# Kernel optimization log

Measured on AMD Instinct MI355X. Metric: run time of the kernel, lower is better.

## Reference

```python
import jax, jax.numpy as jnp
import numpy as np

D_MODEL = 1024
NUM_HEADS = 16
ROPE_THETA = 10000.0


def setup_inputs() -> dict:
    key = jax.random.key(0)
    ks = jax.random.split(key, 5)
    B, S, D = 4, 2048, D_MODEL
    std = (2.0 / (D * D)) ** 0.5
    return {
        "x": jax.random.normal(ks[0], (B, S, D), dtype=jnp.float32),
        "Wq": jax.random.normal(ks[1], (D, D), dtype=jnp.float32) * std,
        "Wk": jax.random.normal(ks[2], (D, D), dtype=jnp.float32) * std,
        "Wv": jax.random.normal(ks[3], (D, D), dtype=jnp.float32) * std,
        "Wo": jax.random.normal(ks[4], (D, D), dtype=jnp.float32) * std,
    }


def _apply_rope(t, sin, cos):
    # t: [B, H, S, d_k]; sin/cos: [S, d_k//2] (broadcast over B, H)
    e = t[..., 0::2]
    o = t[..., 1::2]
    rot = jnp.stack((e * cos - o * sin, e * sin + o * cos), axis=-1)
    return rot.reshape(t.shape)  # interleave back to d_k


def reference(x, Wq, Wk, Wv, Wo):
    B, S, D = x.shape
    H = NUM_HEADS
    dk = D // H

    def proj(W):
        y = jnp.einsum('bsd,ed->bse', x, W)  # Linear: weight is [out, in]
        return y.reshape(B, S, H, dk).transpose(0, 2, 1, 3)  # [B,H,S,dk]

    q, k, v = proj(Wq), proj(Wk), proj(Wv)

    # RoPE cache (token_positions = arange(S))
    half = dk // 2
    inv_freq = 1.0 / (ROPE_THETA ** (jnp.arange(half, dtype=jnp.float32) * 2.0 / dk))
    angles = jnp.arange(S, dtype=jnp.float32)[:, None] * inv_freq[None, :]  # [S, half]
    sin, cos = jnp.sin(angles), jnp.cos(angles)
    q = _apply_rope(q, sin, cos)
    k = _apply_rope(k, sin, cos)

    # scaled dot-product attention with causal mask
    scores = jnp.einsum('bhqd,bhkd->bhqk', q, k) / jnp.sqrt(jnp.float32(dk))
    causal = jnp.tril(jnp.ones((S, S), dtype=bool))
    scores = jnp.where(causal, scores, jnp.finfo(scores.dtype).min)
    p = jax.nn.softmax(scores, axis=-1)
    out = jnp.einsum('bhqk,bhkd->bhqd', p, v)  # [B,H,S,dk]

    out = out.transpose(0, 2, 1, 3).reshape(B, S, D)
    return jnp.einsum('bsd,ed->bse', out, Wo)
```

## Files before the change

### kernel.cpp

```cpp
#include <hip/hip_runtime.h>

typedef unsigned short u16;
typedef unsigned int   u32;

typedef short    short8 __attribute__((ext_vector_type(8)));
typedef __bf16   bf16x8 __attribute__((ext_vector_type(8)));
typedef _Float16 half8  __attribute__((ext_vector_type(8)));
typedef float    f32x4  __attribute__((ext_vector_type(4)));

#define S_LEN   2048
#define DM      1024
#define NHEAD   16
#define DK      64
#define BH_TOT  64
#define M_TOK   8192
#define KDIM    1024

__device__ __forceinline__ u16 f2bf(float f) {
    u32 u = __builtin_bit_cast(u32, f);
    u += 0x7FFFu + ((u >> 16) & 1u);
    return (u16)(u >> 16);
}
__device__ __forceinline__ f32x4 mfma_bf16(short8 a, short8 b, f32x4 c) {
    return __builtin_amdgcn_mfma_f32_16x16x32_bf16(
        __builtin_bit_cast(bf16x8, a), __builtin_bit_cast(bf16x8, b), c, 0, 0, 0);
}
__device__ __forceinline__ f32x4 mfma_f16(half8 a, half8 b, f32x4 c) {
    return __builtin_amdgcn_mfma_f32_16x16x32_f16(a, b, c, 0, 0, 0);
}
__device__ __forceinline__ u32 pk_f16(float a, float b) {
    return __builtin_bit_cast(u32, __builtin_amdgcn_cvt_pkrtz(a, b));
}
__device__ __forceinline__ void gl_lds16(const void* g, void* l) {
    __builtin_amdgcn_global_load_lds(
        (const __attribute__((address_space(1))) u32*)g,
        (__attribute__((address_space(3))) u32*)l, 16, 0, 0);
}
__device__ __forceinline__ void bar_raw() { asm volatile("s_barrier" ::: "memory"); }
__device__ __forceinline__ void wait_vm4() { asm volatile("s_waitcnt vmcnt(4)" ::: "memory"); }
__device__ __forceinline__ void wait_vm0() { asm volatile("s_waitcnt vmcnt(0)" ::: "memory"); }

__device__ __forceinline__ int perm_inv(int rc) {
    const int nt = rc >> 4, mid = (rc >> 2) & 3, r = rc & 3;
    return 32 * (nt >> 1) + 8 * mid + 4 * (nt & 1) + r;
}

__global__ void cvt_all(const float4* __restrict__ x,  const float4* __restrict__ Wq,
                        const float4* __restrict__ Wk, const float4* __restrict__ Wv,
                        const float4* __restrict__ Wo,
                        uint2* __restrict__ oX, uint2* __restrict__ oWcat,
                        uint2* __restrict__ oWo,
                        float* __restrict__ sT, float* __restrict__ cT) {
    const int i = blockIdx.x * 256 + threadIdx.x;
    if (i < 3145728) {
        const float4* in;
        uint2* out;
        if (i < 2097152) {
            in = x + i;  out = oX + i;
        } else {
            const int j = i - 2097152;
            const int w = j >> 18, k = j & 262143;
            in  = (w == 0 ? Wq : w == 1 ? Wk : w == 2 ? Wv : Wo) + k;
            out = (w < 3) ? (oWcat + w * 262144 + k) : (oWo + k);
        }
        float4 f = *in;
        uint2 o;
        o.x = (u32)f2bf(f.x) | ((u32)f2bf(f.y) << 16);
        o.y = (u32)f2bf(f.z) | ((u32)f2bf(f.w) << 16);
        *out = o;
    } else {
        const int idx = i - 3145728;
        const float fi = expf(-(float)(idx >> 11) * 0.287823136624255f);
        const float ang = (float)(idx & 2047) * fi;
        sT[idx] = sinf(ang);
        cT[idx] = cosf(ang);
    }
}

template <int MODE>
__global__ __launch_bounds__(256)
void gemm_nt(const u16* __restrict__ A, const u16* __restrict__ Bw,
             u16* __restrict__ oQ, u16* __restrict__ oK, u16* __restrict__ oVt,
             float* __restrict__ oF,
             const float* __restrict__ ropeS, const float* __restrict__ ropeC) {
    __shared__ u16 As[2][128 * 32];
    __shared__ u16 Bs[2][128 * 32];
    const int tid  = threadIdx.x;
    const int wave = tid >> 6, lane = tid & 63;
    const int quad = lane >> 4, l15 = lane & 15;
    const int wr = wave >> 1, wc = wave & 1;
    const int mbase = blockIdx.y * 128;
    const int nbase = blockIdx.x * 128;

    f32x4 acc[4][4];
#pragma unroll
    for (int i = 0; i < 4; i++)
#pragma unroll
        for (int j = 0; j < 4; j++) acc[i][j] = (f32x4)0.0f;

    const int srow0 = wave * 32 + (lane >> 2);
    const int srow1 = srow0 + 16;
    const int scolb = ((lane & 3) ^ ((lane >> 3) & 3)) * 16;
    const int ldsOff = wave * 2048 + lane * 16;
    const u16* gA0 = A  + (size_t)(mbase + srow0) * KDIM;
    const u16* gA1 = A  + (size_t)(mbase + srow1) * KDIM;
    const u16* gB0 = Bw + (size_t)(nbase + srow0) * KDIM;
    const u16* gB1 = Bw + (size_t)(nbase + srow1) * KDIM;
    const int koffq = (quad ^ ((l15 >> 1) & 3)) * 8;

    gl_lds16((const char*)gA0 + scolb, (char*)As[0] + ldsOff);
    gl_lds16((const char*)gA1 + scolb, (char*)As[0] + ldsOff + 1024);
    gl_lds16((const char*)gB0 + scolb, (char*)Bs[0] + ldsOff);
    gl_lds16((const char*)gB1 + scolb, (char*)Bs[0] + ldsOff + 1024);

    const int KT = KDIM / 32;
    for (int kt = 0; kt < KT; kt++) {
        const int cur = kt & 1, nxt = cur ^ 1;
        const int kkn = ((kt + 1 < KT) ? (kt + 1) : kt) * 32;
        bar_raw();
        gl_lds16((const char*)(gA0 + kkn) + scolb, (char*)As[nxt] + ldsOff);
        gl_lds16((const char*)(gA1 + kkn) + scolb, (char*)As[nxt] + ldsOff + 1024);
        gl_lds16((const char*)(gB0 + kkn) + scolb, (char*)Bs[nxt] + ldsOff);
        gl_lds16((const char*)(gB1 + kkn) + scolb, (char*)Bs[nxt] + ldsOff + 1024);
        wait_vm4();
        bar_raw();

        short8 af[4], bf[4];
#pragma unroll
        for (int mt = 0; mt < 4; mt++)
            af[mt] = *(const short8*)&As[cur][(wr * 64 + mt * 16 + l15) * 32 + koffq];
#pragma unroll
        for (int nt = 0; nt < 4; nt++)
            bf[nt] = *(const short8*)&Bs[cur][(wc * 64 + nt * 16 + l15) * 32 + koffq];
#pragma unroll
        for (int mt = 0; mt < 4; mt++)
#pragma unroll
            for (int nt = 0; nt < 4; nt++)
                acc[mt][nt] = mfma_bf16(af[mt], bf[nt], acc[mt][nt]);
    }
    wait_vm0();

    const int proj_blk = (MODE == 0) ? (nbase >> 10) : 2;

    const float* sB[4];
    const float* cB[4];
    if (MODE == 0 && proj_blk < 2) {
#pragma unroll
        for (int nt = 0; nt < 4; nt++) {
            const int fi = nt * 8 + (l15 >> 1);
            sB[nt] = ropeS + fi * 2048;
            cB[nt] = ropeC + fi * 2048;
        }
    }
    const int par = l15 & 1;

#pragma unroll
    for (int mt = 0; mt < 4; mt++) {
#pragma unroll
        for (int nt = 0; nt < 4; nt++) {
            const int n  = nbase + wc * 64 + nt * 16 + l15;
            const int mb = mbase + wr * 64 + mt * 16 + quad * 4;
            f32x4 v = acc[mt][nt];
            if (MODE == 0) {
                const int e = n & 1023;
                const int h = e >> 6, d = e & 63;
                if (proj_blk == 2) {
                    const int b_ = mb >> 11, s = mb & 2047;
                    const int bh = b_ * NHEAD + h;
                    uint2 pk;
                    pk.x = pk_f16(v[0], v[1]);
                    pk.y = pk_f16(v[2], v[3]);
                    *(uint2*)&oVt[((size_t)bh * DK + d) * S_LEN + s] = pk;
                } else {
                    u16* dst = (proj_blk == 0) ? oQ : oK;
                    float vp[4];
#pragma unroll
                    for (int r = 0; r < 4; r++) vp[r] = __shfl_xor(v[r], 1);
                    const int b_ = mb >> 11, s0 = mb & 2047;
                    const int bh = b_ * NHEAD + h;
                    const f32x4 sn = *(const f32x4*)(sB[nt] + s0);
                    const f32x4 cs = *(const f32x4*)(cB[nt] + s0);
#pragma unroll
                    for (int r = 0; r < 4; r++) {
                        const float res = par ? (vp[r] * sn[r] + v[r] * cs[r])
                                              : (v[r] * cs[r] - vp[r] * sn[r]);
                        dst[((size_t)bh * S_LEN + (s0 + r)) * DK + d] = f2bf(res);
                    }
                }
            } else {
#pragma unroll
                for (int r = 0; r < 4; r++)
                    oF[(size_t)(mb + r) * DM + n] = v[r];
            }
        }
    }
}

__global__ __launch_bounds__(256)
void flash_attn(const u16* __restrict__ Q, const u16* __restrict__ K,
                const u16* __restrict__ Vt, u16* __restrict__ Oc) {
    __shared__ u16 Ks[2][64 * 64];
    __shared__ u16 Vs[2][64 * 64];
    const int qt = 15 - (int)blockIdx.y;
    const int bh = blockIdx.x;
    const int tid  = threadIdx.x;
    const int wave = tid >> 6, lane = tid & 63;
    const int quad = lane >> 4, l15 = lane & 15;
    const int x7 = l15 & 7;
    const size_t headQK = (size_t)bh * S_LEN * DK;
    const size_t headVt = (size_t)bh * DK * S_LEN;
    const int b = bh >> 4, h = bh & 15;
    const float SCL = 0.18033688011112042f;

    half8 ones;
#pragma unroll
    for (int j = 0; j < 8; j++) ones[j] = (_Float16)1.0f;

    const int rwl  = lane >> 3;
    const int scol = (lane & 7) ^ rwl;
    const int rc0 = wave * 16 + rwl, rc1 = rc0 + 8;
    const u16* gK0 = K  + headQK + (size_t)perm_inv(rc0) * DK + scol * 8;
    const u16* gK1 = K  + headQK + (size_t)perm_inv(rc1) * DK + scol * 8;
    const u16* gV0 = Vt + headVt + (size_t)rc0 * S_LEN + scol * 8;
    const u16* gV1 = Vt + headVt + (size_t)rc1 * S_LEN + scol * 8;
    const int ldsOff = wave * 2048 + lane * 16;
    const int koff0 = (quad ^ x7) * 8;
    const int koff1 = ((4 + quad) ^ x7) * 8;

    short8 qf[2][2];
#pragma unroll
    for (int hh = 0; hh < 2; hh++) {
        const int qrow = qt * 128 + hh * 64 + wave * 16 + l15;
        qf[hh][0] = *(const short8*)&Q[headQK + (size_t)qrow * DK + quad * 8];
        qf[hh][1] = *(const short8*)&Q[headQK + (size_t)qrow * DK + 32 + quad * 8];
    }

    float m_st[2];
    f32x4 lacc[2];
    f32x4 oacc[2][4];
#pragma unroll
    for (int hh = 0; hh < 2; hh++) {
        m_st[hh] = -__builtin_inff();
        lacc[hh] = (f32x4)0.0f;
#pragma unroll
        for (int n = 0; n < 4; n++) oacc[hh][n] = (f32x4)0.0f;
    }

    const int NT = 2 * qt + 2;
    gl_lds16(gK0, (char*)Ks[0] + ldsOff);
    gl_lds16(gK1, (char*)Ks[0] + ldsOff + 1024);
    gl_lds16(gV0, (char*)Vs[0] + ldsOff);
    gl_lds16(gV1, (char*)Vs[0] + ldsOff + 1024);

    for (int kt = 0; kt < NT; kt++) {
        const int cur = kt & 1, nxt = cur ^ 1;
        bar_raw();
        {
            const int ktn = (kt + 1 < NT) ? kt + 1 : kt;
            gl_lds16(gK0 + (size_t)ktn * 64 * DK, (char*)Ks[nxt] + ldsOff);
            gl_lds16(gK1 + (size_t)ktn * 64 * DK, (char*)Ks[nxt] + ldsOff + 1024);
            gl_lds16(gV0 + ktn * 64,              (char*)Vs[nxt] + ldsOff);
            gl_lds16(gV1 + ktn * 64,              (char*)Vs[nxt] + ldsOff + 1024);
        }
        wait_vm4();
        bar_raw();

#pragma unroll
        for (int hh = 0; hh < 2; hh++) {
            if (hh == 0 && kt == 2 * qt + 1) continue;
            f32x4 sc[4];
#pragma unroll
            for (int nt = 0; nt < 4; nt++) {
                const int rb = (nt * 16 + l15) * 64;
                short8 kf0 = *(const short8*)&Ks[cur][rb + koff0];
                short8 kf1 = *(const short8*)&Ks[cur][rb + koff1];
                f32x4 z = (f32x4)0.0f;
                z = mfma_bf16(kf0, qf[hh][0], z);
                z = mfma_bf16(kf1, qf[hh][1], z);
#pragma unroll
                for (int r = 0; r < 4; r++) z[r] *= SCL;
                sc[nt] = z;
            }
            if (kt == 2 * qt + hh) {
                const int qloc = wave * 16 + l15;
#pragma unroll
                for (int nt = 0; nt < 4; nt++) {
                    const int kb = 32 * (nt >> 1) + 8 * quad + 4 * (nt & 1);
#pragma unroll
                    for (int r = 0; r < 4; r++)
                        if (kb + r > qloc) sc[nt][r] = -__builtin_inff();
                }
            }
            float mx0 = fmaxf(fmaxf(sc[0][0], sc[0][1]), fmaxf(sc[0][2], sc[0][3]));
            float mx1 = fmaxf(fmaxf(sc[1][0], sc[1][1]), fmaxf(sc[1][2], sc[1][3]));
            float mx2 = fmaxf(fmaxf(sc[2][0], sc[2][1]), fmaxf(sc[2][2], sc[2][3]));
            float mx3 = fmaxf(fmaxf(sc[3][0], sc[3][1]), fmaxf(sc[3][2], sc[3][3]));
            float mx = fmaxf(fmaxf(mx0, mx1), fmaxf(mx2, mx3));
            mx = fmaxf(mx, __shfl_xor(mx, 16));
            mx = fmaxf(mx, __shfl_xor(mx, 32));
            const float mn = fmaxf(m_st[hh], mx);
            const float alpha = __builtin_amdgcn_exp2f(m_st[hh] - mn);
            m_st[hh] = mn;
#pragma unroll
            for (int nt = 0; nt < 4; nt++)
#pragma unroll
                for (int r = 0; r < 4; r++)
                    sc[nt][r] = __builtin_amdgcn_exp2f(sc[nt][r] - m_st[hh]);
            u32 pw[8];
            pw[0] = pk_f16(sc[0][0], sc[0][1]); pw[1] = pk_f16(sc[0][2], sc[0][3]);
            pw[2] = pk_f16(sc[1][0], sc[1][1]); pw[3] = pk_f16(sc[1][2], sc[1][3]);
            pw[4] = pk_f16(sc[2][0], sc[2][1]); pw[5] = pk_f16(sc[2][2], sc[2][3]);
            pw[6] = pk_f16(sc[3][0], sc[3][1]); pw[7] = pk_f16(sc[3][2], sc[3][3]);
            half8 pf0 = __builtin_bit_cast(half8, *(uint4*)&pw[0]);
            half8 pf1 = __builtin_bit_cast(half8, *(uint4*)&pw[4]);
            float alr[4];
#pragma unroll
            for (int r = 0; r < 4; r++) alr[r] = __shfl(alpha, quad * 20 + r);
#pragma unroll
            for (int n = 0; n < 4; n++)
#pragma unroll
                for (int r = 0; r < 4; r++) oacc[hh][n][r] *= alr[r];
#pragma unroll
            for (int r = 0; r < 4; r++) lacc[hh][r] *= alr[r];
#pragma unroll
            for (int c = 0; c < 2; c++) {
                const half8 pf = c ? pf1 : pf0;
                lacc[hh] = mfma_f16(pf, ones, lacc[hh]);
                const int voff = ((c * 4 + quad) ^ x7) * 8;
#pragma unroll
                for (int nt2 = 0; nt2 < 4; nt2++) {
                    half8 vf = __builtin_bit_cast(half8,
                        *(const short8*)&Vs[cur][(nt2 * 16 + l15) * 64 + voff]);
                    oacc[hh][nt2] = mfma_f16(pf, vf, oacc[hh][nt2]);
                }
            }
        }
    }
    wait_vm0();

#pragma unroll
    for (int hh = 0; hh < 2; hh++) {
#pragma unroll
        for (int r = 0; r < 4; r++) {
            const float inv = 1.0f / lacc[hh][r];
            const int s = qt * 128 + hh * 64 + wave * 16 + quad * 4 + r;
#pragma unroll
            for (int nt2 = 0; nt2 < 4; nt2++)
                Oc[((size_t)(b * S_LEN + s)) * DM + h * 64 + nt2 * 16 + l15] =
                    f2bf(oacc[hh][nt2][r] * inv);
        }
    }
}

#define OFF_XBF   ((size_t)0)
#define OFF_WCAT  ((size_t)8388608)
#define OFF_WO    ((size_t)11534336)
#define OFF_QB    ((size_t)12582912)
#define OFF_KB    ((size_t)20971520)
#define OFF_VT    ((size_t)29360128)
#define OFF_ROPE  ((size_t)37748736)

extern "C" void kernel_launch(void* const* d_in, const int* in_sizes, int n_in,
                              void* d_out, int out_size, void* d_ws, size_t ws_size,
                              hipStream_t stream) {
    const float* x  = (const float*)d_in[0];
    const float* Wq = (const float*)d_in[1];
    const float* Wk = (const float*)d_in[2];
    const float* Wv = (const float*)d_in[3];
    const float* Wo = (const float*)d_in[4];
    u16* ws  = (u16*)d_ws;
    u16* XBF = ws + OFF_XBF;
    u16* WCA = ws + OFF_WCAT;
    u16* WOB = ws + OFF_WO;
    u16* QB  = ws + OFF_QB;
    u16* KB  = ws + OFF_KB;
    u16* VT  = ws + OFF_VT;
    float* ropeS = (float*)(ws + OFF_ROPE);
    float* ropeC = ropeS + 65536;
    u16* AT  = XBF;

    cvt_all<<<12544, 256, 0, stream>>>((const float4*)x, (const float4*)Wq,
                                       (const float4*)Wk, (const float4*)Wv,
                                       (const float4*)Wo,
                                       (uint2*)XBF, (uint2*)WCA, (uint2*)WOB,
                                       ropeS, ropeC);

    gemm_nt<0><<<dim3(24, 64), 256, 0, stream>>>(XBF, WCA, QB, KB, VT, nullptr,
                                                 ropeS, ropeC);
    flash_attn<<<dim3(64, 16), 256, 0, stream>>>(QB, KB, VT, AT);
    gemm_nt<1><<<dim3(8, 64), 256, 0, stream>>>(AT, WOB, nullptr, nullptr, nullptr,
                                                (float*)d_out, nullptr, nullptr);
}
```

Measured before the change: 269.4 us.

## Split output GEMM into smaller-tile kernel and interleave flash-attn half-tiles

```diff
diff --git a/kernel.cpp b/kernel.cpp
--- a/kernel.cpp
+++ b/kernel.cpp
@@ -38,6 +38,7 @@
 }
 __device__ __forceinline__ void bar_raw() { asm volatile("s_barrier" ::: "memory"); }
 __device__ __forceinline__ void wait_vm4() { asm volatile("s_waitcnt vmcnt(4)" ::: "memory"); }
+__device__ __forceinline__ void wait_vm3() { asm volatile("s_waitcnt vmcnt(3)" ::: "memory"); }
 __device__ __forceinline__ void wait_vm0() { asm volatile("s_waitcnt vmcnt(0)" ::: "memory"); }
 
 __device__ __forceinline__ int perm_inv(int rc) {
@@ -77,12 +78,10 @@
     }
 }
 
-template <int MODE>
 __global__ __launch_bounds__(256)
-void gemm_nt(const u16* __restrict__ A, const u16* __restrict__ Bw,
-             u16* __restrict__ oQ, u16* __restrict__ oK, u16* __restrict__ oVt,
-             float* __restrict__ oF,
-             const float* __restrict__ ropeS, const float* __restrict__ ropeC) {
+void gemm_qkv(const u16* __restrict__ A, const u16* __restrict__ Bw,
+              u16* __restrict__ oQ, u16* __restrict__ oK, u16* __restrict__ oVt,
+              const float* __restrict__ ropeS, const float* __restrict__ ropeC) {
     __shared__ u16 As[2][128 * 32];
     __shared__ u16 Bs[2][128 * 32];
     const int tid  = threadIdx.x;
@@ -140,11 +139,11 @@
     }
     wait_vm0();
 
-    const int proj_blk = (MODE == 0) ? (nbase >> 10) : 2;
+    const int proj_blk = nbase >> 10;
 
     const float* sB[4];
     const float* cB[4];
-    if (MODE == 0 && proj_blk < 2) {
+    if (proj_blk < 2) {
 #pragma unroll
         for (int nt = 0; nt < 4; nt++) {
             const int fi = nt * 8 + (l15 >> 1);
@@ -161,37 +160,104 @@
             const int n  = nbase + wc * 64 + nt * 16 + l15;
             const int mb = mbase + wr * 64 + mt * 16 + quad * 4;
             f32x4 v = acc[mt][nt];
-            if (MODE == 0) {
-                const int e = n & 1023;
-                const int h = e >> 6, d = e & 63;
-                if (proj_blk == 2) {
-                    const int b_ = mb >> 11, s = mb & 2047;
-                    const int bh = b_ * NHEAD + h;
-                    uint2 pk;
-                    pk.x = pk_f16(v[0], v[1]);
-                    pk.y = pk_f16(v[2], v[3]);
-                    *(uint2*)&oVt[((size_t)bh * DK + d) * S_LEN + s] = pk;
-                } else {
-                    u16* dst = (proj_blk == 0) ? oQ : oK;
-                    float vp[4];
-#pragma unroll
-                    for (int r = 0; r < 4; r++) vp[r] = __shfl_xor(v[r], 1);
-                    const int b_ = mb >> 11, s0 = mb & 2047;
-                    const int bh = b_ * NHEAD + h;
-                    const f32x4 sn = *(const f32x4*)(sB[nt] + s0);
-                    const f32x4 cs = *(const f32x4*)(cB[nt] + s0);
-#pragma unroll
-                    for (int r = 0; r < 4; r++) {
-                        const float res = par ? (vp[r] * sn[r] + v[r] * cs[r])
-                                              : (v[r] * cs[r] - vp[r] * sn[r]);
-                        dst[((size_t)bh * S_LEN + (s0 + r)) * DK + d] = f2bf(res);
-                    }
+            const int e = n & 1023;
+            const int h = e >> 6, d = e & 63;
+            if (proj_blk == 2) {
+                const int b_ = mb >> 11, s = mb & 2047;
+                const int bh = b_ * NHEAD + h;
+                uint2 pk;
+                pk.x = pk_f16(v[0], v[1]);
+                pk.y = pk_f16(v[2], v[3]);
+                *(uint2*)&oVt[((size_t)bh * DK + d) * S_LEN + s] = pk;
+            } else {
+                u16* dst = (proj_blk == 0) ? oQ : oK;
+                float vp[4];
+#pragma unroll
+                for (int r = 0; r < 4; r++) vp[r] = __shfl_xor(v[r], 1);
+                const int b_ = mb >> 11, s0 = mb & 2047;
+                const int bh = b_ * NHEAD + h;
+                const f32x4 sn = *(const f32x4*)(sB[nt] + s0);
+                const f32x4 cs = *(const f32x4*)(cB[nt] + s0);
+#pragma unroll
+                for (int r = 0; r < 4; r++) {
+                    const float res = par ? (vp[r] * sn[r] + v[r] * cs[r])
+                                          : (v[r] * cs[r] - vp[r] * sn[r]);
+                    dst[((size_t)bh * S_LEN + (s0 + r)) * DK + d] = f2bf(res);
                 }
-            } else {
-#pragma unroll
-                for (int r = 0; r < 4; r++)
-                    oF[(size_t)(mb + r) * DM + n] = v[r];
             }
+        }
+    }
+}
+
+__global__ __launch_bounds__(256)
+void gemm_out(const u16* __restrict__ A, const u16* __restrict__ Bw,
+              float* __restrict__ oF) {
+    __shared__ u16 As[2][64 * 32];
+    __shared__ u16 Bs[2][128 * 32];
+    const int tid  = threadIdx.x;
+    const int wave = tid >> 6, lane = tid & 63;
+    const int quad = lane >> 4, l15 = lane & 15;
+    const int wr = wave >> 1, wc = wave & 1;
+    const int mbase = blockIdx.y * 64;
+    const int nbase = blockIdx.x * 128;
+
+    f32x4 acc[2][4];
+#pragma unroll
+    for (int i = 0; i < 2; i++)
+#pragma unroll
+        for (int j = 0; j < 4; j++) acc[i][j] = (f32x4)0.0f;
+
+    const int srowA  = wave * 16 + (lane >> 2);
+    const int srowB0 = wave * 32 + (lane >> 2);
+    const int srowB1 = srowB0 + 16;
+    const int scolb  = ((lane & 3) ^ ((lane >> 3) & 3)) * 16;
+    const int ldsOffA = wave * 1024 + lane * 16;
+    const int ldsOffB = wave * 2048 + lane * 16;
+    const u16* gA  = A  + (size_t)(mbase + srowA)  * KDIM;
+    const u16* gB0 = Bw + (size_t)(nbase + srowB0) * KDIM;
+    const u16* gB1 = Bw + (size_t)(nbase + srowB1) * KDIM;
+    const int koffq = (quad ^ ((l15 >> 1) & 3)) * 8;
+
+    gl_lds16((const char*)gA  + scolb, (char*)As[0] + ldsOffA);
+    gl_lds16((const char*)gB0 + scolb, (char*)Bs[0] + ldsOffB);
+    gl_lds16((const char*)gB1 + scolb, (char*)Bs[0] + ldsOffB + 1024);
+
+    const int KT = KDIM / 32;
+    for (int kt = 0; kt < KT; kt++) {
+        const int cur = kt & 1, nxt = cur ^ 1;
+        const int kkn = ((kt + 1 < KT) ? (kt + 1) : kt) * 32;
+        bar_raw();
+        gl_lds16((const char*)(gA  + kkn) + scolb, (char*)As[nxt] + ldsOffA);
+        gl_lds16((const char*)(gB0 + kkn) + scolb, (char*)Bs[nxt] + ldsOffB);
+        gl_lds16((const char*)(gB1 + kkn) + scolb, (char*)Bs[nxt] + ldsOffB + 1024);
+        wait_vm3();
+        bar_raw();
+
+        short8 af[2], bf[4];
+#pragma unroll
+        for (int mt = 0; mt < 2; mt++)
+            af[mt] = *(const short8*)&As[cur][(wr * 32 + mt * 16 + l15) * 32 + koffq];
+#pragma unroll
+        for (int nt = 0; nt < 4; nt++)
+            bf[nt] = *(const short8*)&Bs[cur][(wc * 64 + nt * 16 + l15) * 32 + koffq];
+#pragma unroll
+        for (int mt = 0; mt < 2; mt++)
+#pragma unroll
+            for (int nt = 0; nt < 4; nt++)
+                acc[mt][nt] = mfma_bf16(af[mt], bf[nt], acc[mt][nt]);
+    }
+    wait_vm0();
+
+#pragma unroll
+    for (int mt = 0; mt < 2; mt++) {
+#pragma unroll
+        for (int nt = 0; nt < 4; nt++) {
+            const int n  = nbase + wc * 64 + nt * 16 + l15;
+            const int mb = mbase + wr * 32 + mt * 16 + quad * 4;
+            f32x4 v = acc[mt][nt];
+#pragma unroll
+            for (int r = 0; r < 4; r++)
+                oF[(size_t)(mb + r) * DM + n] = v[r];
         }
     }
 }
@@ -265,22 +331,26 @@
         wait_vm4();
         bar_raw();
 
-#pragma unroll
-        for (int hh = 0; hh < 2; hh++) {
-            if (hh == 0 && kt == 2 * qt + 1) continue;
-            f32x4 sc[4];
-#pragma unroll
-            for (int nt = 0; nt < 4; nt++) {
-                const int rb = (nt * 16 + l15) * 64;
-                short8 kf0 = *(const short8*)&Ks[cur][rb + koff0];
-                short8 kf1 = *(const short8*)&Ks[cur][rb + koff1];
+        const bool live0 = (kt <= 2 * qt);
+
+        f32x4 sc[2][4];
+#pragma unroll
+        for (int nt = 0; nt < 4; nt++) {
+            const int rb = (nt * 16 + l15) * 64;
+            const short8 kf0 = *(const short8*)&Ks[cur][rb + koff0];
+            const short8 kf1 = *(const short8*)&Ks[cur][rb + koff1];
+#pragma unroll
+            for (int hh = 0; hh < 2; hh++) {
                 f32x4 z = (f32x4)0.0f;
                 z = mfma_bf16(kf0, qf[hh][0], z);
                 z = mfma_bf16(kf1, qf[hh][1], z);
 #pragma unroll
                 for (int r = 0; r < 4; r++) z[r] *= SCL;
-                sc[nt] = z;
+                sc[hh][nt] = z;
             }
+        }
+#pragma unroll
+        for (int hh = 0; hh < 2; hh++) {
             if (kt == 2 * qt + hh) {
                 const int qloc = wave * 16 + l15;
 #pragma unroll
@@ -288,51 +358,64 @@
                     const int kb = 32 * (nt >> 1) + 8 * quad + 4 * (nt & 1);
 #pragma unroll
                     for (int r = 0; r < 4; r++)
-                        if (kb + r > qloc) sc[nt][r] = -__builtin_inff();
+                        if (kb + r > qloc) sc[hh][nt][r] = -__builtin_inff();
                 }
             }
-            float mx0 = fmaxf(fmaxf(sc[0][0], sc[0][1]), fmaxf(sc[0][2], sc[0][3]));
-            float mx1 = fmaxf(fmaxf(sc[1][0], sc[1][1]), fmaxf(sc[1][2], sc[1][3]));
-            float mx2 = fmaxf(fmaxf(sc[2][0], sc[2][1]), fmaxf(sc[2][2], sc[2][3]));
-            float mx3 = fmaxf(fmaxf(sc[3][0], sc[3][1]), fmaxf(sc[3][2], sc[3][3]));
-            float mx = fmaxf(fmaxf(mx0, mx1), fmaxf(mx2, mx3));
-            mx = fmaxf(mx, __shfl_xor(mx, 16));
-            mx = fmaxf(mx, __shfl_xor(mx, 32));
-            const float mn = fmaxf(m_st[hh], mx);
-            const float alpha = __builtin_amdgcn_exp2f(m_st[hh] - mn);
-            m_st[hh] = mn;
-#pragma unroll
-            for (int nt = 0; nt < 4; nt++)
-#pragma unroll
-                for (int r = 0; r < 4; r++)
-                    sc[nt][r] = __builtin_amdgcn_exp2f(sc[nt][r] - m_st[hh]);
-            u32 pw[8];
-            pw[0] = pk_f16(sc[0][0], sc[0][1]); pw[1] = pk_f16(sc[0][2], sc[0][3]);
-            pw[2] = pk_f16(sc[1][0], sc[1][1]); pw[3] = pk_f16(sc[1][2], sc[1][3]);
-            pw[4] = pk_f16(sc[2][0], sc[2][1]); pw[5] = pk_f16(sc[2][2], sc[2][3]);
-            pw[6] = pk_f16(sc[3][0], sc[3][1]); pw[7] = pk_f16(sc[3][2], sc[3][3]);
-            half8 pf0 = __builtin_bit_cast(half8, *(uint4*)&pw[0]);
-            half8 pf1 = __builtin_bit_cast(half8, *(uint4*)&pw[4]);
-            float alr[4];
-#pragma unroll
-            for (int r = 0; r < 4; r++) alr[r] = __shfl(alpha, quad * 20 + r);
-#pragma unroll
-            for (int n = 0; n < 4; n++)
-#pragma unroll
-                for (int r = 0; r < 4; r++) oacc[hh][n][r] *= alr[r];
-#pragma unroll
-            for (int r = 0; r < 4; r++) lacc[hh][r] *= alr[r];
-#pragma unroll
-            for (int c = 0; c < 2; c++) {
-                const half8 pf = c ? pf1 : pf0;
-                lacc[hh] = mfma_f16(pf, ones, lacc[hh]);
-                const int voff = ((c * 4 + quad) ^ x7) * 8;
-#pragma unroll
-                for (int nt2 = 0; nt2 < 4; nt2++) {
-                    half8 vf = __builtin_bit_cast(half8,
-                        *(const short8*)&Vs[cur][(nt2 * 16 + l15) * 64 + voff]);
-                    oacc[hh][nt2] = mfma_f16(pf, vf, oacc[hh][nt2]);
-                }
+        }
+        half8 pf[2][2];
+        float alr[2][4];
+#pragma unroll
+        for (int hh = 0; hh < 2; hh++) {
+            const bool live = (hh == 1) || live0;
+            if (live) {
+                float mx0 = fmaxf(fmaxf(sc[hh][0][0], sc[hh][0][1]), fmaxf(sc[hh][0][2], sc[hh][0][3]));
+                float mx1 = fmaxf(fmaxf(sc[hh][1][0], sc[hh][1][1]), fmaxf(sc[hh][1][2], sc[hh][1][3]));
+                float mx2 = fmaxf(fmaxf(sc[hh][2][0], sc[hh][2][1]), fmaxf(sc[hh][2][2], sc[hh][2][3]));
+                float mx3 = fmaxf(fmaxf(sc[hh][3][0], sc[hh][3][1]), fmaxf(sc[hh][3][2], sc[hh][3][3]));
+                float mx = fmaxf(fmaxf(mx0, mx1), fmaxf(mx2, mx3));
+                mx = fmaxf(mx, __shfl_xor(mx, 16));
+                mx = fmaxf(mx, __shfl_xor(mx, 32));
+                const float mn = fmaxf(m_st[hh], mx);
+                const float alpha = __builtin_amdgcn_exp2f(m_st[hh] - mn);
+                m_st[hh] = mn;
+#pragma unroll
+                for (int nt = 0; nt < 4; nt++)
+#pragma unroll
+                    for (int r = 0; r < 4; r++)
+                        sc[hh][nt][r] = __builtin_amdgcn_exp2f(sc[hh][nt][r] - mn);
+                u32 pw[8];
+                pw[0] = pk_f16(sc[hh][0][0], sc[hh][0][1]); pw[1] = pk_f16(sc[hh][0][2], sc[hh][0][3]);
+                pw[2] = pk_f16(sc[hh][1][0], sc[hh][1][1]); pw[3] = pk_f16(sc[hh][1][2], sc[hh][1][3]);
+                pw[4] = pk_f16(sc[hh][2][0], sc[hh][2][1]); pw[5] = pk_f16(sc[hh][2][2], sc[hh][2][3]);
+                pw[6] = pk_f16(sc[hh][3][0], sc[hh][3][1]); pw[7] = pk_f16(sc[hh][3][2], sc[hh][3][3]);
+                pf[hh][0] = __builtin_bit_cast(half8, *(uint4*)&pw[0]);
+                pf[hh][1] = __builtin_bit_cast(half8, *(uint4*)&pw[4]);
+                float alv[4];
+#pragma unroll
+                for (int r = 0; r < 4; r++) alv[r] = __shfl(alpha, quad * 20 + r);
+#pragma unroll
+                for (int n = 0; n < 4; n++)
+#pragma unroll
+                    for (int r = 0; r < 4; r++) oacc[hh][n][r] *= alv[r];
+#pragma unroll
+                for (int r = 0; r < 4; r++) lacc[hh][r] *= alv[r];
+                (void)alr;
+            } else {
+                pf[hh][0] = (half8)(_Float16)0.0f;
+                pf[hh][1] = (half8)(_Float16)0.0f;
+            }
+        }
+#pragma unroll
+        for (int c = 0; c < 2; c++) {
+            lacc[0] = mfma_f16(pf[0][c], ones, lacc[0]);
+            lacc[1] = mfma_f16(pf[1][c], ones, lacc[1]);
+            const int voff = ((c * 4 + quad) ^ x7) * 8;
+#pragma unroll
+            for (int nt2 = 0; nt2 < 4; nt2++) {
+                const half8 vf = __builtin_bit_cast(half8,
+                    *(const short8*)&Vs[cur][(nt2 * 16 + l15) * 64 + voff]);
+                oacc[0][nt2] = mfma_f16(pf[0][c], vf, oacc[0][nt2]);
+                oacc[1][nt2] = mfma_f16(pf[1][c], vf, oacc[1][nt2]);
             }
         }
     }
@@ -385,9 +468,7 @@
                                        (uint2*)XBF, (uint2*)WCA, (uint2*)WOB,
                                        ropeS, ropeC);
 
-    gemm_nt<0><<<dim3(24, 64), 256, 0, stream>>>(XBF, WCA, QB, KB, VT, nullptr,
-                                                 ropeS, ropeC);
+    gemm_qkv<<<dim3(24, 64), 256, 0, stream>>>(XBF, WCA, QB, KB, VT, ropeS, ropeC);
     flash_attn<<<dim3(64, 16), 256, 0, stream>>>(QB, KB, VT, AT);
-    gemm_nt<1><<<dim3(8, 64), 256, 0, stream>>>(AT, WOB, nullptr, nullptr, nullptr,
-                                                (float*)d_out, nullptr, nullptr);
-}
+    gemm_out<<<dim3(8, 128), 256, 0, stream>>>(AT, WOB, (float*)d_out);
+}
```

After: 281.8 us. 1.05x slower.
